# Kernel tuning notes

Hardware: AMD Instinct MI355X
Metric: run time of the kernel (lower is better)

Reference implementation:

```python
import jax, jax.numpy as jnp
import numpy as np

N = 8192
E = 262144
EMBED = 128
EDGE_DIM = 16
EPS = 1e-09
SLOPE = 0.01  # LeakyReLU default


def leaky_relu(x):
    return jnp.where(x >= 0, x, SLOPE * x)


def setup_inputs() -> dict:
    key = jax.random.key(0)
    ks = jax.random.split(key, 12)
    x = jax.random.randint(ks[0], (N, 1), 0, 20, dtype=jnp.int64)
    edge_index = jax.random.randint(ks[1], (2, E), 0, N, dtype=jnp.int64)
    edge_attr = jax.random.normal(ks[2], (E, EDGE_DIM), dtype=jnp.float32)
    emb = jax.random.normal(ks[3], (20, EMBED), dtype=jnp.float32)
    # conv1: nn = Linear(EMBED, 64); edge lin: EDGE_DIM -> EMBED
    W1 = jax.random.normal(ks[4], (EMBED, 64), dtype=jnp.float32) * 0.05
    b1 = jnp.zeros((64,), dtype=jnp.float32)
    E1w = jax.random.normal(ks[5], (EDGE_DIM, EMBED), dtype=jnp.float32) * 0.1
    E1b = jnp.zeros((EMBED,), dtype=jnp.float32)
    # conv6: nn = Linear(64, 32); edge lin: EDGE_DIM -> 64
    W2 = jax.random.normal(ks[6], (64, 32), dtype=jnp.float32) * 0.05
    b2 = jnp.zeros((32,), dtype=jnp.float32)
    E2w = jax.random.normal(ks[7], (EDGE_DIM, 64), dtype=jnp.float32) * 0.1
    E2b = jnp.zeros((64,), dtype=jnp.float32)
    return {"x": x, "edge_index": edge_index, "edge_attr": edge_attr,
            "emb": emb, "W1": W1, "b1": b1, "E1w": E1w, "E1b": E1b,
            "W2": W2, "b2": b2, "E2w": E2w, "E2b": E2b}


def gine_conv(h, src, dst, edge_emb, W, b):
    # message: relu(h[src] + edge_emb); aggregate: scatter-add at dst
    m = jax.nn.relu(h[src] + edge_emb)                      # [E, d]
    agg = jax.ops.segment_sum(m, dst, num_segments=N)       # [N, d]
    return ((1.0 + EPS) * h + agg) @ W + b


def reference(x, edge_index, edge_attr, emb, W1, b1, E1w, E1b, W2, b2, E2w, E2b):
    h = emb[x[:, 0]]                                         # [N, EMBED]
    src, dst = edge_index[0], edge_index[1]
    h = gine_conv(h, src, dst, edge_attr @ E1w + E1b, W1, b1)  # [N, 64]
    h = leaky_relu(h)
    h = gine_conv(h, src, dst, edge_attr @ E2w + E2b, W2, b2)  # [N, 32]
    return h @ h.T                                           # [N, N]
```

## Files before the change

### kernel.cpp

```cpp
#include <hip/hip_runtime.h>
#include <hip/hip_bf16.h>

#define NN 8192
#define NE 262144
#define EPSF 1e-9f

typedef __attribute__((ext_vector_type(8))) short short8;
typedef __attribute__((ext_vector_type(4))) float floatx4;

__global__ __launch_bounds__(256) void embed_deg_kernel(const int* __restrict__ x,
    const float* __restrict__ emb, float* __restrict__ h0,
    const int* __restrict__ ei, int* __restrict__ deg) {
  int tid = blockIdx.x * 256 + threadIdx.x;
  int n = tid >> 5, j = tid & 31;
  int xi = x[n];
  ((float4*)h0)[(size_t)n * 32 + j] = ((const float4*)emb)[xi * 32 + j];
  atomicAdd(&deg[ei[NE + tid]], 1);
}

__global__ __launch_bounds__(256) void scan_kernel(const int* __restrict__ deg,
    int* __restrict__ rowptr, int* __restrict__ cursor) {
  __shared__ int wsum[4];
  int t = threadIdx.x;
  int lane = t & 63, w = t >> 6;
  int base = t * 32;
  int local[32];
  int s = 0;
#pragma unroll
  for (int i = 0; i < 32; ++i) { local[i] = deg[base + i]; s += local[i]; }
  int sc = s;
#pragma unroll
  for (int d = 1; d < 64; d <<= 1) {
    int v = __shfl_up(sc, d);
    if (lane >= d) sc += v;
  }
  if (lane == 63) wsum[w] = sc;
  __syncthreads();
  int woff = 0;
  for (int u = 0; u < w; ++u) woff += wsum[u];
  int run = woff + sc - s;
#pragma unroll
  for (int i = 0; i < 32; ++i) {
    rowptr[base + i] = run;
    cursor[base + i] = run;
    run += local[i];
  }
  if (t == 255) rowptr[NN] = run;
}

__global__ __launch_bounds__(256) void scatter_kernel(const int* __restrict__ ei,
    int* __restrict__ cursor, int2* __restrict__ csr) {
  int e = blockIdx.x * 256 + threadIdx.x;
  int s = ei[e], d = ei[NE + e];
  int pos = atomicAdd(&cursor[d], 1);
  csr[pos] = (int2){e, s};
}

__global__ __launch_bounds__(256) void fused1_kernel(const int* __restrict__ rowptr,
    const int2* __restrict__ csr, const float* __restrict__ ea,
    const float* __restrict__ E1w, const float* __restrict__ E1b,
    const float* __restrict__ W1, const float* __restrict__ b1,
    const float* __restrict__ h0, float* __restrict__ h1) {
  __shared__ float sE[16 * 128];
  __shared__ float sEb[128];
  __shared__ float st[4][128];
  for (int i = threadIdx.x; i < 16 * 128; i += 256) sE[i] = E1w[i];
  if (threadIdx.x < 128) sEb[threadIdx.x] = E1b[threadIdx.x];
  __syncthreads();
  int lane = threadIdx.x & 63;
  int w = threadIdx.x >> 6;
  int n = blockIdx.x * 4 + w;
  int beg = rowptr[n], end = rowptr[n + 1];
  float acc0 = 0.f, acc1 = 0.f;
  int i = beg;
  int2 pa, pb;
  bool have = (i + 2 <= end);
  if (have) { pa = csr[i]; pb = csr[i + 1]; }
  while (have) {
    int eA = __builtin_amdgcn_readfirstlane(pa.x);
    int sA = __builtin_amdgcn_readfirstlane(pa.y);
    int eB = __builtin_amdgcn_readfirstlane(pb.x);
    int sB = __builtin_amdgcn_readfirstlane(pb.y);
    float hA0 = h0[(size_t)sA * 128 + lane];
    float hA1 = h0[(size_t)sA * 128 + lane + 64];
    float hB0 = h0[(size_t)sB * 128 + lane];
    float hB1 = h0[(size_t)sB * 128 + lane + 64];
    i += 2;
    have = (i + 2 <= end);
    if (have) { pa = csr[i]; pb = csr[i + 1]; }
    const float* eaA = ea + (size_t)eA * 16;
    const float* eaB = ea + (size_t)eB * 16;
    float eeA0 = sEb[lane], eeA1 = sEb[lane + 64];
    float eeB0 = eeA0, eeB1 = eeA1;
#pragma unroll
    for (int k = 0; k < 16; ++k) {
      float w0 = sE[k * 128 + lane], w1 = sE[k * 128 + lane + 64];
      eeA0 += eaA[k] * w0; eeA1 += eaA[k] * w1;
      eeB0 += eaB[k] * w0; eeB1 += eaB[k] * w1;
    }
    float mA0 = hA0 + eeA0, mA1 = hA1 + eeA1;
    float mB0 = hB0 + eeB0, mB1 = hB1 + eeB1;
    acc0 += (mA0 > 0.f ? mA0 : 0.f) + (mB0 > 0.f ? mB0 : 0.f);
    acc1 += (mA1 > 0.f ? mA1 : 0.f) + (mB1 > 0.f ? mB1 : 0.f);
  }
  for (; i < end; ++i) {
    int2 p = csr[i];
    int e = __builtin_amdgcn_readfirstlane(p.x);
    int s = __builtin_amdgcn_readfirstlane(p.y);
    float h_0 = h0[(size_t)s * 128 + lane];
    float h_1 = h0[(size_t)s * 128 + lane + 64];
    const float* eav = ea + (size_t)e * 16;
    float ee0 = sEb[lane], ee1 = sEb[lane + 64];
#pragma unroll
    for (int k = 0; k < 16; ++k) {
      ee0 += eav[k] * sE[k * 128 + lane];
      ee1 += eav[k] * sE[k * 128 + lane + 64];
    }
    float m0 = h_0 + ee0, m1 = h_1 + ee1;
    acc0 += m0 > 0.f ? m0 : 0.f;
    acc1 += m1 > 0.f ? m1 : 0.f;
  }
  st[w][lane]      = (1.0f + EPSF) * h0[(size_t)n * 128 + lane] + acc0;
  st[w][lane + 64] = (1.0f + EPSF) * h0[(size_t)n * 128 + lane + 64] + acc1;
  float o = b1[lane];
#pragma unroll 16
  for (int k = 0; k < 128; ++k) o += st[w][k] * W1[k * 64 + lane];
  h1[(size_t)n * 64 + lane] = o > 0.f ? o : 0.01f * o;
}

__global__ __launch_bounds__(256) void fused2_kernel(const int* __restrict__ rowptr,
    const int2* __restrict__ csr, const float* __restrict__ ea,
    const float* __restrict__ E2w, const float* __restrict__ E2b,
    const float* __restrict__ W2, const float* __restrict__ b2,
    const float* __restrict__ h1, short* __restrict__ h2) {
  __shared__ float sE[16 * 64];
  __shared__ float sEb[64];
  __shared__ float st[4][64];
  for (int i = threadIdx.x; i < 16 * 64; i += 256) sE[i] = E2w[i];
  if (threadIdx.x < 64) sEb[threadIdx.x] = E2b[threadIdx.x];
  __syncthreads();
  int lane = threadIdx.x & 63;
  int w = threadIdx.x >> 6;
  int n = blockIdx.x * 4 + w;
  int beg = rowptr[n], end = rowptr[n + 1];
  float acc = 0.f;
  int i = beg;
  int2 pa, pb;
  bool have = (i + 2 <= end);
  if (have) { pa = csr[i]; pb = csr[i + 1]; }
  while (have) {
    int eA = __builtin_amdgcn_readfirstlane(pa.x);
    int sA = __builtin_amdgcn_readfirstlane(pa.y);
    int eB = __builtin_amdgcn_readfirstlane(pb.x);
    int sB = __builtin_amdgcn_readfirstlane(pb.y);
    float hA = h1[(size_t)sA * 64 + lane];
    float hB = h1[(size_t)sB * 64 + lane];
    i += 2;
    have = (i + 2 <= end);
    if (have) { pa = csr[i]; pb = csr[i + 1]; }
    const float* eaA = ea + (size_t)eA * 16;
    const float* eaB = ea + (size_t)eB * 16;
    float eeA = sEb[lane], eeB = eeA;
#pragma unroll
    for (int k = 0; k < 16; ++k) {
      float wv = sE[k * 64 + lane];
      eeA += eaA[k] * wv;
      eeB += eaB[k] * wv;
    }
    float mA = hA + eeA, mB = hB + eeB;
    acc += (mA > 0.f ? mA : 0.f) + (mB > 0.f ? mB : 0.f);
  }
  for (; i < end; ++i) {
    int2 p = csr[i];
    int e = __builtin_amdgcn_readfirstlane(p.x);
    int s = __builtin_amdgcn_readfirstlane(p.y);
    float hv = h1[(size_t)s * 64 + lane];
    const float* eav = ea + (size_t)e * 16;
    float ee = sEb[lane];
#pragma unroll
    for (int k = 0; k < 16; ++k) ee += eav[k] * sE[k * 64 + lane];
    float m = hv + ee;
    acc += m > 0.f ? m : 0.f;
  }
  st[w][lane] = (1.0f + EPSF) * h1[(size_t)n * 64 + lane] + acc;
  int col = lane & 31;
  float o = b2[col];
#pragma unroll 16
  for (int k = 0; k < 64; ++k) o += st[w][k] * W2[k * 32 + col];
  if (lane < 32) {
    unsigned u = __builtin_bit_cast(unsigned, o);
    u += 0x7fffu + ((u >> 16) & 1u);
    h2[(size_t)n * 32 + col] = (short)(u >> 16);
  }
}

__global__ __launch_bounds__(256) void gemm_kernel(const short* __restrict__ h2,
    float* __restrict__ out) {
  int wid = (blockIdx.x * 256 + threadIdx.x) >> 6;
  int lane = threadIdx.x & 63;
  int cg = wid & 127;
  int rt = wid >> 7;
  int r = lane & 15, q = lane >> 4;
  short8 afrag = *(const short8*)(h2 + ((rt * 16 + r) * 32 + q * 8));
  floatx4 acc[4];
#pragma unroll
  for (int t = 0; t < 4; ++t) {
    short8 bfrag = *(const short8*)(h2 + ((cg * 64 + t * 16 + r) * 32 + q * 8));
    floatx4 z = {0.f, 0.f, 0.f, 0.f};
    acc[t] = __builtin_amdgcn_mfma_f32_16x16x32_bf16(afrag, bfrag, z, 0, 0, 0);
  }
  int row_base = rt * 16 + q * 4;
  int col_base = cg * 64 + r;
#pragma unroll
  for (int t = 0; t < 4; ++t)
#pragma unroll
    for (int reg = 0; reg < 4; ++reg)
      out[(size_t)(row_base + reg) * NN + col_base + t * 16] = acc[t][reg];
}

extern "C" void kernel_launch(void* const* d_in, const int* in_sizes, int n_in,
                              void* d_out, int out_size, void* d_ws, size_t ws_size,
                              hipStream_t stream) {
  const int*   x   = (const int*)d_in[0];
  const int*   ei  = (const int*)d_in[1];
  const float* ea  = (const float*)d_in[2];
  const float* emb = (const float*)d_in[3];
  const float* W1  = (const float*)d_in[4];
  const float* b1  = (const float*)d_in[5];
  const float* E1w = (const float*)d_in[6];
  const float* E1b = (const float*)d_in[7];
  const float* W2  = (const float*)d_in[8];
  const float* b2  = (const float*)d_in[9];
  const float* E2w = (const float*)d_in[10];
  const float* E2b = (const float*)d_in[11];

  float* ws     = (float*)d_ws;
  float* h0     = ws;
  float* h1     = ws + 1048576;
  short* h2     = (short*)(ws + 1572864);
  int*   deg    = (int*)(ws + 1703936);
  int*   rowptr = (int*)(ws + 1712128);
  int*   cursor = (int*)(ws + 1720832);
  int2*  csr    = (int2*)(ws + 1729024);

  hipMemsetAsync(deg, 0, NN * sizeof(int), stream);
  embed_deg_kernel<<<1024, 256, 0, stream>>>(x, emb, h0, ei, deg);
  scan_kernel<<<1, 256, 0, stream>>>(deg, rowptr, cursor);
  scatter_kernel<<<1024, 256, 0, stream>>>(ei, cursor, csr);
  fused1_kernel<<<2048, 256, 0, stream>>>(rowptr, csr, ea, E1w, E1b, W1, b1, h0, h1);
  fused2_kernel<<<2048, 256, 0, stream>>>(rowptr, csr, ea, E2w, E2b, W2, b2, h1, h2);
  gemm_kernel<<<16384, 256, 0, stream>>>(h2, (float*)d_out);
}
```

Baseline: 380.1 us.

## Prefetch edge attrs as float4, pack edge weights, stage GEMM output via LDS

The fused GINE kernels now load each edge's 16 attributes as four float4 loads, one iteration ahead of use, instead of scalar loads inside the FMA loop. The edge-weight matrix in shared memory is interleaved so each lane reads a float2 per step. The final 8192x8192 GEMM writes its MFMA tiles through a per-wave padded LDS buffer, so global stores become row-contiguous float4 writes instead of scattered scalar stores. This adds register pressure and LDS use in exchange for fewer, wider memory transactions, mainly on the large output write.

```diff
diff --git a/kernel.cpp b/kernel.cpp
--- a/kernel.cpp
+++ b/kernel.cpp
@@ -61,10 +61,13 @@
     const float* __restrict__ E1w, const float* __restrict__ E1b,
     const float* __restrict__ W1, const float* __restrict__ b1,
     const float* __restrict__ h0, float* __restrict__ h1) {
-  __shared__ float sE[16 * 128];
+  __shared__ float sEp[16 * 128];
   __shared__ float sEb[128];
   __shared__ float st[4][128];
-  for (int i = threadIdx.x; i < 16 * 128; i += 256) sE[i] = E1w[i];
+  for (int i = threadIdx.x; i < 16 * 128; i += 256) {
+    int k = i >> 7, c = i & 127;
+    sEp[k * 128 + (c & 63) * 2 + (c >> 6)] = E1w[i];
+  }
   if (threadIdx.x < 128) sEb[threadIdx.x] = E1b[threadIdx.x];
   __syncthreads();
   int lane = threadIdx.x & 63;
@@ -74,29 +77,46 @@
   float acc0 = 0.f, acc1 = 0.f;
   int i = beg;
   int2 pa, pb;
+  float4 A0, A1, A2, A3, B0, B1, B2, B3;
   bool have = (i + 2 <= end);
-  if (have) { pa = csr[i]; pb = csr[i + 1]; }
+  if (have) {
+    pa = csr[i]; pb = csr[i + 1];
+    int eA = __builtin_amdgcn_readfirstlane(pa.x);
+    int eB = __builtin_amdgcn_readfirstlane(pb.x);
+    const float4* qa = (const float4*)(ea + (size_t)eA * 16);
+    const float4* qb = (const float4*)(ea + (size_t)eB * 16);
+    A0 = qa[0]; A1 = qa[1]; A2 = qa[2]; A3 = qa[3];
+    B0 = qb[0]; B1 = qb[1]; B2 = qb[2]; B3 = qb[3];
+  }
   while (have) {
-    int eA = __builtin_amdgcn_readfirstlane(pa.x);
     int sA = __builtin_amdgcn_readfirstlane(pa.y);
-    int eB = __builtin_amdgcn_readfirstlane(pb.x);
     int sB = __builtin_amdgcn_readfirstlane(pb.y);
     float hA0 = h0[(size_t)sA * 128 + lane];
     float hA1 = h0[(size_t)sA * 128 + lane + 64];
     float hB0 = h0[(size_t)sB * 128 + lane];
     float hB1 = h0[(size_t)sB * 128 + lane + 64];
+    float cA[16] = {A0.x, A0.y, A0.z, A0.w, A1.x, A1.y, A1.z, A1.w,
+                    A2.x, A2.y, A2.z, A2.w, A3.x, A3.y, A3.z, A3.w};
+    float cB[16] = {B0.x, B0.y, B0.z, B0.w, B1.x, B1.y, B1.z, B1.w,
+                    B2.x, B2.y, B2.z, B2.w, B3.x, B3.y, B3.z, B3.w};
     i += 2;
     have = (i + 2 <= end);
-    if (have) { pa = csr[i]; pb = csr[i + 1]; }
-    const float* eaA = ea + (size_t)eA * 16;
-    const float* eaB = ea + (size_t)eB * 16;
+    if (have) {
+      pa = csr[i]; pb = csr[i + 1];
+      int eA = __builtin_amdgcn_readfirstlane(pa.x);
+      int eB = __builtin_amdgcn_readfirstlane(pb.x);
+      const float4* qa = (const float4*)(ea + (size_t)eA * 16);
+      const float4* qb = (const float4*)(ea + (size_t)eB * 16);
+      A0 = qa[0]; A1 = qa[1]; A2 = qa[2]; A3 = qa[3];
+      B0 = qb[0]; B1 = qb[1]; B2 = qb[2]; B3 = qb[3];
+    }
     float eeA0 = sEb[lane], eeA1 = sEb[lane + 64];
     float eeB0 = eeA0, eeB1 = eeA1;
 #pragma unroll
     for (int k = 0; k < 16; ++k) {
-      float w0 = sE[k * 128 + lane], w1 = sE[k * 128 + lane + 64];
-      eeA0 += eaA[k] * w0; eeA1 += eaA[k] * w1;
-      eeB0 += eaB[k] * w0; eeB1 += eaB[k] * w1;
+      float2 wv = *(const float2*)&sEp[k * 128 + lane * 2];
+      eeA0 += cA[k] * wv.x; eeA1 += cA[k] * wv.y;
+      eeB0 += cB[k] * wv.x; eeB1 += cB[k] * wv.y;
     }
     float mA0 = hA0 + eeA0, mA1 = hA1 + eeA1;
     float mB0 = hB0 + eeB0, mB1 = hB1 + eeB1;
@@ -113,8 +133,9 @@
     float ee0 = sEb[lane], ee1 = sEb[lane + 64];
 #pragma unroll
     for (int k = 0; k < 16; ++k) {
-      ee0 += eav[k] * sE[k * 128 + lane];
-      ee1 += eav[k] * sE[k * 128 + lane + 64];
+      float2 wv = *(const float2*)&sEp[k * 128 + lane * 2];
+      ee0 += eav[k] * wv.x;
+      ee1 += eav[k] * wv.y;
     }
     float m0 = h_0 + ee0, m1 = h_1 + ee1;
     acc0 += m0 > 0.f ? m0 : 0.f;
@@ -133,10 +154,13 @@
     const float* __restrict__ E2w, const float* __restrict__ E2b,
     const float* __restrict__ W2, const float* __restrict__ b2,
     const float* __restrict__ h1, short* __restrict__ h2) {
-  __shared__ float sE[16 * 64];
+  __shared__ float sEp[8 * 128];
   __shared__ float sEb[64];
   __shared__ float st[4][64];
-  for (int i = threadIdx.x; i < 16 * 64; i += 256) sE[i] = E2w[i];
+  for (int i = threadIdx.x; i < 16 * 64; i += 256) {
+    int k = i >> 6, c = i & 63;
+    sEp[(k >> 1) * 128 + c * 2 + (k & 1)] = E2w[i];
+  }
   if (threadIdx.x < 64) sEb[threadIdx.x] = E2b[threadIdx.x];
   __syncthreads();
   int lane = threadIdx.x & 63;
@@ -146,26 +170,45 @@
   float acc = 0.f;
   int i = beg;
   int2 pa, pb;
+  float4 A0, A1, A2, A3, B0, B1, B2, B3;
   bool have = (i + 2 <= end);
-  if (have) { pa = csr[i]; pb = csr[i + 1]; }
+  if (have) {
+    pa = csr[i]; pb = csr[i + 1];
+    int eA = __builtin_amdgcn_readfirstlane(pa.x);
+    int eB = __builtin_amdgcn_readfirstlane(pb.x);
+    const float4* qa = (const float4*)(ea + (size_t)eA * 16);
+    const float4* qb = (const float4*)(ea + (size_t)eB * 16);
+    A0 = qa[0]; A1 = qa[1]; A2 = qa[2]; A3 = qa[3];
+    B0 = qb[0]; B1 = qb[1]; B2 = qb[2]; B3 = qb[3];
+  }
   while (have) {
-    int eA = __builtin_amdgcn_readfirstlane(pa.x);
     int sA = __builtin_amdgcn_readfirstlane(pa.y);
-    int eB = __builtin_amdgcn_readfirstlane(pb.x);
     int sB = __builtin_amdgcn_readfirstlane(pb.y);
     float hA = h1[(size_t)sA * 64 + lane];
     float hB = h1[(size_t)sB * 64 + lane];
+    float cA[16] = {A0.x, A0.y, A0.z, A0.w, A1.x, A1.y, A1.z, A1.w,
+                    A2.x, A2.y, A2.z, A2.w, A3.x, A3.y, A3.z, A3.w};
+    float cB[16] = {B0.x, B0.y, B0.z, B0.w, B1.x, B1.y, B1.z, B1.w,
+                    B2.x, B2.y, B2.z, B2.w, B3.x, B3.y, B3.z, B3.w};
     i += 2;
     have = (i + 2 <= end);
-    if (have) { pa = csr[i]; pb = csr[i + 1]; }
-    const float* eaA = ea + (size_t)eA * 16;
-    const float* eaB = ea + (size_t)eB * 16;
+    if (have) {
+      pa = csr[i]; pb = csr[i + 1];
+      int eA = __builtin_amdgcn_readfirstlane(pa.x);
+      int eB = __builtin_amdgcn_readfirstlane(pb.x);
+      const float4* qa = (const float4*)(ea + (size_t)eA * 16);
+      const float4* qb = (const float4*)(ea + (size_t)eB * 16);
+      A0 = qa[0]; A1 = qa[1]; A2 = qa[2]; A3 = qa[3];
+      B0 = qb[0]; B1 = qb[1]; B2 = qb[2]; B3 = qb[3];
+    }
     float eeA = sEb[lane], eeB = eeA;
 #pragma unroll
-    for (int k = 0; k < 16; ++k) {
-      float wv = sE[k * 64 + lane];
-      eeA += eaA[k] * wv;
-      eeB += eaB[k] * wv;
+    for (int k2 = 0; k2 < 8; ++k2) {
+      float2 wv = *(const float2*)&sEp[k2 * 128 + lane * 2];
+      eeA += cA[2 * k2] * wv.x;
+      eeA += cA[2 * k2 + 1] * wv.y;
+      eeB += cB[2 * k2] * wv.x;
+      eeB += cB[2 * k2 + 1] * wv.y;
     }
     float mA = hA + eeA, mB = hB + eeB;
     acc += (mA > 0.f ? mA : 0.f) + (mB > 0.f ? mB : 0.f);
@@ -178,7 +221,11 @@
     const float* eav = ea + (size_t)e * 16;
     float ee = sEb[lane];
 #pragma unroll
-    for (int k = 0; k < 16; ++k) ee += eav[k] * sE[k * 64 + lane];
+    for (int k2 = 0; k2 < 8; ++k2) {
+      float2 wv = *(const float2*)&sEp[k2 * 128 + lane * 2];
+      ee += eav[2 * k2] * wv.x;
+      ee += eav[2 * k2 + 1] * wv.y;
+    }
     float m = hv + ee;
     acc += m > 0.f ? m : 0.f;
   }
@@ -196,8 +243,10 @@
 
 __global__ __launch_bounds__(256) void gemm_kernel(const short* __restrict__ h2,
     float* __restrict__ out) {
+  __shared__ float tile[4][16 * 68];
   int wid = (blockIdx.x * 256 + threadIdx.x) >> 6;
   int lane = threadIdx.x & 63;
+  int w = threadIdx.x >> 6;
   int cg = wid & 127;
   int rt = wid >> 7;
   int r = lane & 15, q = lane >> 4;
@@ -209,13 +258,17 @@
     floatx4 z = {0.f, 0.f, 0.f, 0.f};
     acc[t] = __builtin_amdgcn_mfma_f32_16x16x32_bf16(afrag, bfrag, z, 0, 0, 0);
   }
-  int row_base = rt * 16 + q * 4;
-  int col_base = cg * 64 + r;
+  float* T = tile[w];
 #pragma unroll
   for (int t = 0; t < 4; ++t)
 #pragma unroll
     for (int reg = 0; reg < 4; ++reg)
-      out[(size_t)(row_base + reg) * NN + col_base + t * 16] = acc[t][reg];
+      T[(q * 4 + reg) * 68 + t * 16 + r] = acc[t][reg];
+#pragma unroll
+  for (int j = 0; j < 4; ++j) {
+    float4 v = *(const float4*)&T[(j * 4 + q) * 68 + r * 4];
+    *(float4*)&out[(size_t)(rt * 16 + j * 4 + q) * NN + cg * 64 + r * 4] = v;
+  }
 }
 
 extern "C" void kernel_launch(void* const* d_in, const int* in_sizes, int n_in,
```

New measurement: 435.3 us. 14.5% more time.
